# Kernel tuning notes

Hardware: AMD Instinct MI355X
Metric: run time of the kernel (lower is better)

Reference implementation:

```python
import jax, jax.numpy as jnp
import numpy as np

B, S, J, D = 64, 2048, 25, 3
FEAT_DIM = 128
COMPUTED = 12  # pos(3) + vel(3) + acc(3) + angles(3)
IN_MLP = COMPUTED * J  # 300
HID = FEAT_DIM * 2     # 256
CONN = np.array([(0, 1), (1, 5), (1, 6), (5, 7), (7, 9), (6, 8), (8, 10),
                 (1, 11), (1, 12), (11, 13), (13, 15), (12, 14), (14, 16)], dtype=np.int32)


def setup_inputs() -> dict:
    key = jax.random.key(0)
    ks = jax.random.split(key, 8)
    return {
        "poses": jax.random.normal(ks[0], (B, S, J, D), dtype=jnp.float32),
        "W1": jax.random.normal(ks[1], (IN_MLP, HID), dtype=jnp.float32) * 0.05,
        "b1": jnp.zeros((HID,), jnp.float32),
        "gamma": jnp.ones((HID,), jnp.float32),
        "beta": jnp.zeros((HID,), jnp.float32),
        "running_mean": jnp.zeros((HID,), jnp.float32),
        "running_var": jnp.ones((HID,), jnp.float32),
        "W2": jax.random.normal(ks[2], (HID, FEAT_DIM), dtype=jnp.float32) * 0.05,
        "b2": jnp.zeros((FEAT_DIM,), jnp.float32),
        "joint_weights": jnp.ones((J,), jnp.float32),
    }


def reference(poses, W1, b1, gamma, beta, running_mean, running_var, W2, b2, joint_weights):
    b, s, j, d = poses.shape
    # --- root-centering + max-distance normalization ---
    p = poses - poses[:, :, 0:1, :]
    dist = jnp.linalg.norm(p, axis=-1, keepdims=True)           # [B,S,J,1]
    max_dist = jnp.max(dist, axis=2, keepdims=True)             # [B,S,1,1]
    p = p / (max_dist + 1e-8)
    # --- velocity / acceleration (zero-padded first frames) ---
    zpad = jnp.zeros_like(p[:, :1])
    vel = jnp.concatenate([zpad, p[:, 1:] - p[:, :-1]], axis=1)
    acc = jnp.concatenate([zpad, vel[:, 1:] - vel[:, :-1]], axis=1)
    # --- joint angles: vectorized gather + normalize + acos (replaces B*S*13 python loop) ---
    v1 = p[:, :, CONN[:, 1], :] - p[:, :, CONN[:, 0], :]        # [B,S,13,3]
    vnorm = jnp.maximum(jnp.linalg.norm(v1, axis=-1, keepdims=True), 1e-12)  # F.normalize eps
    ang = jnp.arccos(jnp.clip(v1 / vnorm, -1.0, 1.0))           # [B,S,13,3]
    ang = ang.reshape(b, s, -1)                                 # [B,S,39]
    pad = jnp.zeros((b, s, j * 3 - ang.shape[-1]), ang.dtype)   # pad to J*3=75
    angles = jnp.concatenate([ang, pad], axis=-1).reshape(b, s, j, 3)
    # --- combine, weight, project ---
    feat = jnp.concatenate([p, vel, acc, angles], axis=-1)      # [B,S,J,12]
    feat = feat * joint_weights.reshape(1, 1, j, 1)
    x = feat.reshape(b * s, -1)                                 # [B*S,300]
    x = x @ W1 + b1
    x = gamma * (x - running_mean) / jnp.sqrt(running_var + 1e-5) + beta  # BN eval mode
    x = jax.nn.relu(x)                                          # dropout = identity (eval)
    x = x @ W2 + b2
    return x.reshape(b, s, -1)                                  # [B,S,128]
```

## Files before the change

kernel.cpp:

```cpp
#include <hip/hip_runtime.h>
#include <hip/hip_bf16.h>
#include <stdint.h>


#define S_    2048
#define MT_   64
#define TPB   512
#define HID_  256
#define OUT_  128

typedef __attribute__((ext_vector_type(8))) short   short8;
typedef __attribute__((ext_vector_type(4))) float   floatx4;

#define C0M 0x0ECDB118675110ULL
#define C1M 0x0FDECBA9786540ULL

__device__ __forceinline__ unsigned short bf16_bits(float v) {
    union { float f; unsigned u; } x; x.f = v;
    unsigned r = x.u + 0x7fffu + ((x.u >> 16) & 1u);
    return (unsigned short)(r >> 16);
}

__device__ __forceinline__ unsigned pkbf16(float a, float b) {
#if __has_builtin(__builtin_amdgcn_cvt_pk_bf16_f32)
    auto v = __builtin_amdgcn_cvt_pk_bf16_f32(a, b);
    unsigned u; __builtin_memcpy(&u, &v, 4); return u;
#else
    return (unsigned)bf16_bits(a) | ((unsigned)bf16_bits(b) << 16);
#endif
}

__device__ __forceinline__ float facos(float x) {
    float ax = fabsf(x);
    float p = fmaf(ax, -0.0187293f, 0.0742610f);
    p = fmaf(ax, p, -0.2121144f);
    p = fmaf(ax, p, 1.5707288f);
    float r = __builtin_amdgcn_sqrtf(1.f - ax) * p;
    return x < 0.f ? 3.14159265358979f - r : r;
}

__global__ void prep_kernel(const float* __restrict__ W1, const float* __restrict__ b1,
                            const float* __restrict__ gamma, const float* __restrict__ beta,
                            const float* __restrict__ rmean, const float* __restrict__ rvar,
                            const float* __restrict__ W2,
                            unsigned short* __restrict__ w1p,
                            unsigned short* __restrict__ w2p,
                            float* __restrict__ b1p) {
    int idx = blockIdx.x * 256 + threadIdx.x;
    if (idx < 81920) {
        int k = idx >> 8, n = idx & 255;
        float a = gamma[n] * __builtin_amdgcn_rsqf(rvar[n] + 1e-5f);
        float v = (k < 300) ? W1[k * HID_ + n] * a : 0.f;
        int blk = (k >> 5) * 16 + (n >> 4);
        int off = blk * 512 + (((k >> 3) & 3) * 16 + (n & 15)) * 8 + (k & 7);
        w1p[off] = bf16_bits(v);
    } else if (idx < 114688) {
        int i2 = idx - 81920;
        int k = i2 >> 7, n = i2 & 127;
        int blk = (k >> 5) * 8 + (n >> 4);
        int off = blk * 512 + (((k >> 3) & 3) * 16 + (n & 15)) * 8 + (k & 7);
        w2p[off] = bf16_bits(W2[k * OUT_ + n]);
    } else if (idx < 114944) {
        int n = idx - 114688;
        float a = gamma[n] * __builtin_amdgcn_rsqf(rvar[n] + 1e-5f);
        b1p[n] = fmaf(a, b1[n] - rmean[n], beta[n]);
    }
}

#define LDS_FEAT 0
#define LDS_PM   41984
#define LDS_RS   43312
#define LDS_JW   (LDS_RS + 66 * 16)
#define LDS_TOT  (LDS_JW + 25 * 4 + 12)

__global__ __launch_bounds__(TPB, 6) void pose_mlp(
    const float* __restrict__ poses,
    const unsigned short* __restrict__ w1p,
    const unsigned short* __restrict__ w2p,
    const float* __restrict__ b1p,
    const float* __restrict__ b2,
    const float* __restrict__ jw,
    float* __restrict__ out)
{
    __shared__ __align__(16) unsigned char smem[LDS_TOT];
    const int tid  = threadIdx.x;
    const int lane = tid & 63;
    const int wv   = tid >> 6;
    const int t0   = blockIdx.x * MT_;
    const int s0   = t0 & (S_ - 1);

    unsigned short* feat = (unsigned short*)(smem + LDS_FEAT);
    float*  pm  = (float*)(smem + LDS_PM);
    float4* rs  = (float4*)(smem + LDS_RS);
    float*  jwl = (float*)(smem + LDS_JW);

    short8 bw[2];
    #pragma unroll
    for (int ni = 0; ni < 2; ni++)
        bw[ni] = *(const short8*)(w1p + (unsigned)(wv * 2 + ni) * 512 + lane * 8);

    if (tid < 25) jwl[tid] = jw[tid];
    for (int i = tid; i < MT_ * 64; i += TPB) {
        int tt = i >> 6, z = i & 63;
        int k;
        if (z < 36) { int jj = z / 3; k = (13 + jj) * 12 + 9 + (z - jj * 3); }
        else        { k = 300 + z - 36; }
        feat[tt * 328 + k] = 0;
    }

    for (int i = tid; i < 66 * 5; i += TPB) {
        int f = i / 5, grp = i - f * 5;
        int g = t0 - 2 + f; if (g < 0) g = 0;
        const float* P = poses + (size_t)g * 75;
        float r0 = P[0], r1 = P[1], r2 = P[2];
        float m2 = 0.f;
        #pragma unroll
        for (int jj = 0; jj < 5; jj++) {
            int j = grp * 5 + jj;
            float dx = P[j*3]   - r0;
            float dy = P[j*3+1] - r1;
            float dz = P[j*3+2] - r2;
            m2 = fmaxf(m2, fmaf(dx, dx, fmaf(dy, dy, dz * dz)));
        }
        pm[i] = m2;
    }
    __syncthreads();
    if (tid < 66) {
        int g = t0 - 2 + tid; if (g < 0) g = 0;
        const float* P = poses + (size_t)g * 75;
        const float* q = pm + tid * 5;
        float m2 = fmaxf(fmaxf(fmaxf(q[0], q[1]), fmaxf(q[2], q[3])), q[4]);
        float sc = __builtin_amdgcn_rcpf(__builtin_amdgcn_sqrtf(m2) + 1e-8f);
        rs[tid] = make_float4(P[0], P[1], P[2], sc);
    }
    __syncthreads();

    for (int i = tid; i < MT_ * 25; i += TPB) {
        int tt = i / 25, j = i - tt * 25;
        int s  = s0 + tt;
        int g  = t0 + tt;
        int g1 = g - 1 < 0 ? 0 : g - 1;
        int g2 = g - 2 < 0 ? 0 : g - 2;
        const float* Pc = poses + (size_t)g  * 75 + j * 3;
        const float* P1 = poses + (size_t)g1 * 75 + j * 3;
        const float* P2 = poses + (size_t)g2 * 75 + j * 3;
        float4 rc = rs[tt + 2], rm = rs[tt + 1], rp = rs[tt];
        float cx = (Pc[0] - rc.x) * rc.w, cy = (Pc[1] - rc.y) * rc.w, cz = (Pc[2] - rc.z) * rc.w;
        float mx = (P1[0] - rm.x) * rm.w, my = (P1[1] - rm.y) * rm.w, mz = (P1[2] - rm.z) * rm.w;
        float px = (P2[0] - rp.x) * rp.w, py = (P2[1] - rp.y) * rp.w, pz = (P2[2] - rp.z) * rp.w;
        bool h1 = (s >= 1), h2 = (s >= 2);
        float vx = h1 ? cx - mx : 0.f, vy = h1 ? cy - my : 0.f, vz = h1 ? cz - mz : 0.f;
        float ux = h2 ? mx - px : 0.f, uy = h2 ? my - py : 0.f, uz = h2 ? mz - pz : 0.f;
        float qx = vx - ux, qy = vy - uy, qz = vz - uz;
        float w = jwl[j];
        unsigned base = (unsigned)tt * 328 + j * 12;
        *(unsigned*)(feat + base)     = pkbf16(cx * w, cy * w);
        *(unsigned*)(feat + base + 2) = pkbf16(cz * w, vx * w);
        *(unsigned*)(feat + base + 4) = pkbf16(vy * w, vz * w);
        *(unsigned*)(feat + base + 6) = pkbf16(qx * w, qy * w);
        feat[base + 8] = bf16_bits(qz * w);
    }

    for (int i = tid; i < MT_ * 13; i += TPB) {
        int tt = i / 13, e = i - tt * 13;
        int g  = t0 + tt;
        const float* P = poses + (size_t)g * 75;
        int a0 = (int)((C0M >> (4 * e)) & 15) * 3;
        int a1 = (((int)((C1M >> (4 * e)) & 15)) + 1) * 3;
        float vx = P[a1] - P[a0], vy = P[a1+1] - P[a0+1], vz = P[a1+2] - P[a0+2];
        float d  = fmaf(vx, vx, fmaf(vy, vy, vz * vz));
        float inv = __builtin_amdgcn_rcpf(fmaxf(__builtin_amdgcn_sqrtf(d), 1e-12f));
        float w = jwl[e];
        float A0 = facos(fminf(fmaxf(vx * inv, -1.f), 1.f)) * w;
        float A1 = facos(fminf(fmaxf(vy * inv, -1.f), 1.f)) * w;
        float A2 = facos(fminf(fmaxf(vz * inv, -1.f), 1.f)) * w;
        unsigned base = (unsigned)tt * 328 + e * 12 + 9;
        feat[base] = bf16_bits(A0);
        *(unsigned*)(feat + base + 1) = pkbf16(A1, A2);
    }
    __syncthreads();

    floatx4 acc[4][2];
    #pragma unroll
    for (int mi = 0; mi < 4; mi++)
        #pragma unroll
        for (int ni = 0; ni < 2; ni++) acc[mi][ni] = (floatx4){0.f, 0.f, 0.f, 0.f};

    #pragma unroll 1
    for (int kc = 0; kc < 10; kc++) {
        short8 bn[2];
        if (kc < 9) {
            #pragma unroll
            for (int ni = 0; ni < 2; ni++)
                bn[ni] = *(const short8*)(w1p + (unsigned)((kc + 1) * 16 + wv * 2 + ni) * 512 + lane * 8);
        }
        short8 af[4];
        #pragma unroll
        for (int mi = 0; mi < 4; mi++)
            af[mi] = *(const short8*)(feat + (mi * 16 + (lane & 15)) * 328 + kc * 32 + (lane >> 4) * 8);
        #pragma unroll
        for (int mi = 0; mi < 4; mi++)
            #pragma unroll
            for (int ni = 0; ni < 2; ni++)
                acc[mi][ni] = __builtin_amdgcn_mfma_f32_16x16x32_bf16(
                    af[mi], bw[ni], acc[mi][ni], 0, 0, 0);
        if (kc < 9) {
            #pragma unroll
            for (int ni = 0; ni < 2; ni++) bw[ni] = bn[ni];
        }
    }

    short8 bw2 = *(const short8*)(w2p + (unsigned)wv * 512 + lane * 8);

    __syncthreads();

    unsigned short* hid = feat;
    float bv[2];
    #pragma unroll
    for (int ni = 0; ni < 2; ni++) bv[ni] = b1p[wv * 32 + ni * 16 + (lane & 15)];
    #pragma unroll
    for (int mi = 0; mi < 4; mi++)
        #pragma unroll
        for (int ni = 0; ni < 2; ni++)
            #pragma unroll
            for (int r = 0; r < 4; r++) {
                float v = fmaxf(acc[mi][ni][r] + bv[ni], 0.f);
                int m   = mi * 16 + (lane >> 4) * 4 + r;
                int col = wv * 32 + ni * 16 + (lane & 15);
                hid[m * 264 + col] = bf16_bits(v);
            }
    __syncthreads();

    floatx4 acc2[4];
    #pragma unroll
    for (int mi = 0; mi < 4; mi++) acc2[mi] = (floatx4){0.f, 0.f, 0.f, 0.f};

    #pragma unroll 1
    for (int kc = 0; kc < 8; kc++) {
        short8 bn2;
        if (kc < 7)
            bn2 = *(const short8*)(w2p + (unsigned)((kc + 1) * 8 + wv) * 512 + lane * 8);
        short8 af[4];
        #pragma unroll
        for (int mi = 0; mi < 4; mi++)
            af[mi] = *(const short8*)(hid + (mi * 16 + (lane & 15)) * 264 + kc * 32 + (lane >> 4) * 8);
        #pragma unroll
        for (int mi = 0; mi < 4; mi++)
            acc2[mi] = __builtin_amdgcn_mfma_f32_16x16x32_bf16(
                af[mi], bw2, acc2[mi], 0, 0, 0);
        if (kc < 7) bw2 = bn2;
    }

    float c2 = b2[wv * 16 + (lane & 15)];
    #pragma unroll
    for (int mi = 0; mi < 4; mi++)
        #pragma unroll
        for (int r = 0; r < 4; r++) {
            int m   = mi * 16 + (lane >> 4) * 4 + r;
            int col = wv * 16 + (lane & 15);
            out[(size_t)(t0 + m) * OUT_ + col] = acc2[mi][r] + c2;
        }
}

extern "C" void kernel_launch(void* const* d_in, const int* in_sizes, int n_in,
                              void* d_out, int out_size, void* d_ws, size_t ws_size,
                              hipStream_t stream) {
    (void)in_sizes; (void)n_in; (void)out_size; (void)ws_size;
    const float* poses = (const float*)d_in[0];
    const float* W1    = (const float*)d_in[1];
    const float* b1    = (const float*)d_in[2];
    const float* gamma = (const float*)d_in[3];
    const float* beta  = (const float*)d_in[4];
    const float* rmean = (const float*)d_in[5];
    const float* rvar  = (const float*)d_in[6];
    const float* W2    = (const float*)d_in[7];
    const float* b2    = (const float*)d_in[8];
    const float* jw    = (const float*)d_in[9];

    unsigned short* w1p = (unsigned short*)d_ws;
    unsigned short* w2p = w1p + 320 * HID_;
    float* b1p = (float*)((char*)d_ws + (320 * HID_ + HID_ * OUT_) * 2);

    prep_kernel<<<449, 256, 0, stream>>>(W1, b1, gamma, beta, rmean, rvar, W2,
                                         w1p, w2p, b1p);
    pose_mlp<<<2048, TPB, 0, stream>>>(poses, w1p, w2p, b1p, b2, jw, (float*)d_out);
}
```

Measured before the change: 144.4 us.

## Fold velocity/acceleration and joint weights into W1, feed shifted normalized poses

Velocity and acceleration are linear in the normalized positions of the current and two previous frames, so their W1 rows are folded into three combined weight groups. The GEMM now reads time-shifted rows of a compact normalized-pose tile. Joint weights are also moved into the weight prep. This removes per-element vel/acc feature construction and shrinks the LDS footprint, allowing 8 blocks per CU instead of 6. The cost is K growing from 320 to 352 (11 MFMA k-chunks instead of 10). Zero-padding at sequence starts is now reproduced by clamping to the first frame, so the differences come out as zero.

```diff
diff --git a/kernel.cpp b/kernel.cpp
--- a/kernel.cpp
+++ b/kernel.cpp
@@ -8,6 +8,7 @@
 #define TPB   512
 #define HID_  256
 #define OUT_  128
+#define NK1   11
 
 typedef __attribute__((ext_vector_type(8))) short   short8;
 typedef __attribute__((ext_vector_type(4))) float   floatx4;
@@ -42,44 +43,63 @@
 __global__ void prep_kernel(const float* __restrict__ W1, const float* __restrict__ b1,
                             const float* __restrict__ gamma, const float* __restrict__ beta,
                             const float* __restrict__ rmean, const float* __restrict__ rvar,
-                            const float* __restrict__ W2,
+                            const float* __restrict__ W2, const float* __restrict__ jw,
                             unsigned short* __restrict__ w1p,
                             unsigned short* __restrict__ w2p,
                             float* __restrict__ b1p) {
     int idx = blockIdx.x * 256 + threadIdx.x;
-    if (idx < 81920) {
+    if (idx < 352 * 256) {
         int k = idx >> 8, n = idx & 255;
         float a = gamma[n] * __builtin_amdgcn_rsqf(rvar[n] + 1e-5f);
-        float v = (k < 300) ? W1[k * HID_ + n] * a : 0.f;
+        float v = 0.f;
+        if (k < 288) {
+            int g = k / 96, kk = k - g * 96;
+            if (kk < 75) {
+                int j = kk / 3, c = kk - j * 3;
+                int base = (j * 12 + c) * HID_ + n;
+                float wp = W1[base];
+                float wv = W1[base + 3 * HID_];
+                float wa = W1[base + 6 * HID_];
+                float m  = jw[j] * a;
+                v = (g == 0 ? (wp + wv + wa) : (g == 1 ? -(wv + 2.f * wa) : wa)) * m;
+            }
+        } else {
+            int kk = k - 288;
+            if (kk < 39) {
+                int j = kk / 3, c = kk - j * 3;
+                v = W1[(j * 12 + 9 + c) * HID_ + n] * jw[j] * a;
+            }
+        }
         int blk = (k >> 5) * 16 + (n >> 4);
         int off = blk * 512 + (((k >> 3) & 3) * 16 + (n & 15)) * 8 + (k & 7);
         w1p[off] = bf16_bits(v);
-    } else if (idx < 114688) {
-        int i2 = idx - 81920;
+    } else if (idx < 352 * 256 + 256 * 128) {
+        int i2 = idx - 352 * 256;
         int k = i2 >> 7, n = i2 & 127;
         int blk = (k >> 5) * 8 + (n >> 4);
         int off = blk * 512 + (((k >> 3) & 3) * 16 + (n & 15)) * 8 + (k & 7);
         w2p[off] = bf16_bits(W2[k * OUT_ + n]);
-    } else if (idx < 114944) {
-        int n = idx - 114688;
+    } else if (idx < 352 * 256 + 256 * 128 + 256) {
+        int n = idx - (352 * 256 + 256 * 128);
         float a = gamma[n] * __builtin_amdgcn_rsqf(rvar[n] + 1e-5f);
         b1p[n] = fmaf(a, b1[n] - rmean[n], beta[n]);
     }
 }
 
-#define LDS_FEAT 0
-#define LDS_PM   41984
-#define LDS_RS   43312
-#define LDS_JW   (LDS_RS + 66 * 16)
-#define LDS_TOT  (LDS_JW + 25 * 4 + 12)
-
-__global__ __launch_bounds__(TPB, 6) void pose_mlp(
+#define PT_STR   100
+#define ANG_STR  72
+#define HID_STR  268
+#define LDS_ANG  13216
+#define LDS_PM   22432
+#define LDS_RS   23760
+#define LDS_TOT  (64 * HID_STR * 2)
+
+__global__ __launch_bounds__(TPB, 8) void pose_mlp(
     const float* __restrict__ poses,
     const unsigned short* __restrict__ w1p,
     const unsigned short* __restrict__ w2p,
     const float* __restrict__ b1p,
     const float* __restrict__ b2,
-    const float* __restrict__ jw,
     float* __restrict__ out)
 {
     __shared__ __align__(16) unsigned char smem[LDS_TOT];
@@ -89,28 +109,19 @@
     const int t0   = blockIdx.x * MT_;
     const int s0   = t0 & (S_ - 1);
 
-    unsigned short* feat = (unsigned short*)(smem + LDS_FEAT);
-    float*  pm  = (float*)(smem + LDS_PM);
-    float4* rs  = (float4*)(smem + LDS_RS);
-    float*  jwl = (float*)(smem + LDS_JW);
+    unsigned short* pt  = (unsigned short*)smem;
+    unsigned short* ang = (unsigned short*)(smem + LDS_ANG);
+    float*  pm = (float*)(smem + LDS_PM);
+    float4* rs = (float4*)(smem + LDS_RS);
 
     short8 bw[2];
     #pragma unroll
     for (int ni = 0; ni < 2; ni++)
         bw[ni] = *(const short8*)(w1p + (unsigned)(wv * 2 + ni) * 512 + lane * 8);
 
-    if (tid < 25) jwl[tid] = jw[tid];
-    for (int i = tid; i < MT_ * 64; i += TPB) {
-        int tt = i >> 6, z = i & 63;
-        int k;
-        if (z < 36) { int jj = z / 3; k = (13 + jj) * 12 + 9 + (z - jj * 3); }
-        else        { k = 300 + z - 36; }
-        feat[tt * 328 + k] = 0;
-    }
-
     for (int i = tid; i < 66 * 5; i += TPB) {
         int f = i / 5, grp = i - f * 5;
-        int g = t0 - 2 + f; if (g < 0) g = 0;
+        int g = (s0 - 2 + f < 0) ? t0 : t0 - 2 + f;
         const float* P = poses + (size_t)g * 75;
         float r0 = P[0], r1 = P[1], r2 = P[2];
         float m2 = 0.f;
@@ -126,7 +137,7 @@
     }
     __syncthreads();
     if (tid < 66) {
-        int g = t0 - 2 + tid; if (g < 0) g = 0;
+        int g = (s0 - 2 + tid < 0) ? t0 : t0 - 2 + tid;
         const float* P = poses + (size_t)g * 75;
         const float* q = pm + tid * 5;
         float m2 = fmaxf(fmaxf(fmaxf(q[0], q[1]), fmaxf(q[2], q[3])), q[4]);
@@ -135,48 +146,46 @@
     }
     __syncthreads();
 
-    for (int i = tid; i < MT_ * 25; i += TPB) {
-        int tt = i / 25, j = i - tt * 25;
-        int s  = s0 + tt;
-        int g  = t0 + tt;
-        int g1 = g - 1 < 0 ? 0 : g - 1;
-        int g2 = g - 2 < 0 ? 0 : g - 2;
-        const float* Pc = poses + (size_t)g  * 75 + j * 3;
-        const float* P1 = poses + (size_t)g1 * 75 + j * 3;
-        const float* P2 = poses + (size_t)g2 * 75 + j * 3;
-        float4 rc = rs[tt + 2], rm = rs[tt + 1], rp = rs[tt];
-        float cx = (Pc[0] - rc.x) * rc.w, cy = (Pc[1] - rc.y) * rc.w, cz = (Pc[2] - rc.z) * rc.w;
-        float mx = (P1[0] - rm.x) * rm.w, my = (P1[1] - rm.y) * rm.w, mz = (P1[2] - rm.z) * rm.w;
-        float px = (P2[0] - rp.x) * rp.w, py = (P2[1] - rp.y) * rp.w, pz = (P2[2] - rp.z) * rp.w;
-        bool h1 = (s >= 1), h2 = (s >= 2);
-        float vx = h1 ? cx - mx : 0.f, vy = h1 ? cy - my : 0.f, vz = h1 ? cz - mz : 0.f;
-        float ux = h2 ? mx - px : 0.f, uy = h2 ? my - py : 0.f, uz = h2 ? mz - pz : 0.f;
-        float qx = vx - ux, qy = vy - uy, qz = vz - uz;
-        float w = jwl[j];
-        unsigned base = (unsigned)tt * 328 + j * 12;
-        *(unsigned*)(feat + base)     = pkbf16(cx * w, cy * w);
-        *(unsigned*)(feat + base + 2) = pkbf16(cz * w, vx * w);
-        *(unsigned*)(feat + base + 4) = pkbf16(vy * w, vz * w);
-        *(unsigned*)(feat + base + 6) = pkbf16(qx * w, qy * w);
-        feat[base + 8] = bf16_bits(qz * w);
+    for (int i = tid; i < 66 * 50; i += TPB) {
+        int f = i / 50, p = i - f * 50;
+        int r0 = 2 * p, r1 = r0 + 1;
+        int g = (s0 - 2 + f < 0) ? t0 : t0 - 2 + f;
+        const float* P = poses + (size_t)g * 75;
+        float4 R = rs[f];
+        float v0 = 0.f, v1 = 0.f;
+        if (r0 < 75) {
+            int c = r0 - (r0 / 3) * 3;
+            float rt = (c == 0) ? R.x : ((c == 1) ? R.y : R.z);
+            v0 = (P[r0] - rt) * R.w;
+        }
+        if (r1 < 75) {
+            int c = r1 - (r1 / 3) * 3;
+            float rt = (c == 0) ? R.x : ((c == 1) ? R.y : R.z);
+            v1 = (P[r1] - rt) * R.w;
+        }
+        *(unsigned*)(pt + f * PT_STR + r0) = pkbf16(v0, v1);
     }
 
     for (int i = tid; i < MT_ * 13; i += TPB) {
         int tt = i / 13, e = i - tt * 13;
-        int g  = t0 + tt;
-        const float* P = poses + (size_t)g * 75;
+        const float* P = poses + (size_t)(t0 + tt) * 75;
         int a0 = (int)((C0M >> (4 * e)) & 15) * 3;
         int a1 = (((int)((C1M >> (4 * e)) & 15)) + 1) * 3;
         float vx = P[a1] - P[a0], vy = P[a1+1] - P[a0+1], vz = P[a1+2] - P[a0+2];
         float d  = fmaf(vx, vx, fmaf(vy, vy, vz * vz));
         float inv = __builtin_amdgcn_rcpf(fmaxf(__builtin_amdgcn_sqrtf(d), 1e-12f));
-        float w = jwl[e];
-        float A0 = facos(fminf(fmaxf(vx * inv, -1.f), 1.f)) * w;
-        float A1 = facos(fminf(fmaxf(vy * inv, -1.f), 1.f)) * w;
-        float A2 = facos(fminf(fmaxf(vz * inv, -1.f), 1.f)) * w;
-        unsigned base = (unsigned)tt * 328 + e * 12 + 9;
-        feat[base] = bf16_bits(A0);
-        *(unsigned*)(feat + base + 1) = pkbf16(A1, A2);
+        float A0 = facos(fminf(fmaxf(vx * inv, -1.f), 1.f));
+        float A1 = facos(fminf(fmaxf(vy * inv, -1.f), 1.f));
+        float A2 = facos(fminf(fmaxf(vz * inv, -1.f), 1.f));
+        unsigned base = (unsigned)tt * ANG_STR + e * 3;
+        ang[base]     = bf16_bits(A0);
+        ang[base + 1] = bf16_bits(A1);
+        ang[base + 2] = bf16_bits(A2);
+    }
+    for (int i = tid; i < MT_ * 13; i += TPB) {
+        int r = i / 13, q = i - r * 13;
+        if (q == 0) ang[r * ANG_STR + 39] = 0;
+        else *(unsigned*)(ang + r * ANG_STR + 40 + 2 * (q - 1)) = 0;
     }
     __syncthreads();
 
@@ -187,24 +196,35 @@
         for (int ni = 0; ni < 2; ni++) acc[mi][ni] = (floatx4){0.f, 0.f, 0.f, 0.f};
 
     #pragma unroll 1
-    for (int kc = 0; kc < 10; kc++) {
+    for (int kc = 0; kc < NK1; kc++) {
         short8 bn[2];
-        if (kc < 9) {
+        if (kc < NK1 - 1) {
             #pragma unroll
             for (int ni = 0; ni < 2; ni++)
                 bn[ni] = *(const short8*)(w1p + (unsigned)((kc + 1) * 16 + wv * 2 + ni) * 512 + lane * 8);
         }
         short8 af[4];
-        #pragma unroll
-        for (int mi = 0; mi < 4; mi++)
-            af[mi] = *(const short8*)(feat + (mi * 16 + (lane & 15)) * 328 + kc * 32 + (lane >> 4) * 8);
+        if (kc < 9) {
+            int grp = kc / 3;
+            int ko  = (kc - grp * 3) * 32 + (lane >> 4) * 8;
+            #pragma unroll
+            for (int mi = 0; mi < 4; mi++) {
+                int row = mi * 16 + (lane & 15) + 2 - grp;
+                af[mi] = *(const short8*)(pt + row * PT_STR + ko);
+            }
+        } else {
+            int ko = (kc - 9) * 32 + (lane >> 4) * 8;
+            #pragma unroll
+            for (int mi = 0; mi < 4; mi++)
+                af[mi] = *(const short8*)(ang + (mi * 16 + (lane & 15)) * ANG_STR + ko);
+        }
         #pragma unroll
         for (int mi = 0; mi < 4; mi++)
             #pragma unroll
             for (int ni = 0; ni < 2; ni++)
                 acc[mi][ni] = __builtin_amdgcn_mfma_f32_16x16x32_bf16(
                     af[mi], bw[ni], acc[mi][ni], 0, 0, 0);
-        if (kc < 9) {
+        if (kc < NK1 - 1) {
             #pragma unroll
             for (int ni = 0; ni < 2; ni++) bw[ni] = bn[ni];
         }
@@ -214,7 +234,7 @@
 
     __syncthreads();
 
-    unsigned short* hid = feat;
+    unsigned short* hid = (unsigned short*)smem;
     float bv[2];
     #pragma unroll
     for (int ni = 0; ni < 2; ni++) bv[ni] = b1p[wv * 32 + ni * 16 + (lane & 15)];
@@ -227,7 +247,7 @@
                 float v = fmaxf(acc[mi][ni][r] + bv[ni], 0.f);
                 int m   = mi * 16 + (lane >> 4) * 4 + r;
                 int col = wv * 32 + ni * 16 + (lane & 15);
-                hid[m * 264 + col] = bf16_bits(v);
+                hid[m * HID_STR + col] = bf16_bits(v);
             }
     __syncthreads();
 
@@ -243,7 +263,7 @@
         short8 af[4];
         #pragma unroll
         for (int mi = 0; mi < 4; mi++)
-            af[mi] = *(const short8*)(hid + (mi * 16 + (lane & 15)) * 264 + kc * 32 + (lane >> 4) * 8);
+            af[mi] = *(const short8*)(hid + (mi * 16 + (lane & 15)) * HID_STR + kc * 32 + (lane >> 4) * 8);
         #pragma unroll
         for (int mi = 0; mi < 4; mi++)
             acc2[mi] = __builtin_amdgcn_mfma_f32_16x16x32_bf16(
@@ -278,10 +298,10 @@
     const float* jw    = (const float*)d_in[9];
 
     unsigned short* w1p = (unsigned short*)d_ws;
-    unsigned short* w2p = w1p + 320 * HID_;
-    float* b1p = (float*)((char*)d_ws + (320 * HID_ + HID_ * OUT_) * 2);
-
-    prep_kernel<<<449, 256, 0, stream>>>(W1, b1, gamma, beta, rmean, rvar, W2,
+    unsigned short* w2p = w1p + 352 * HID_;
+    float* b1p = (float*)((char*)d_ws + (352 * HID_ + HID_ * OUT_) * 2);
+
+    prep_kernel<<<481, 256, 0, stream>>>(W1, b1, gamma, beta, rmean, rvar, W2, jw,
                                          w1p, w2p, b1p);
-    pose_mlp<<<2048, TPB, 0, stream>>>(poses, w1p, w2p, b1p, b2, jw, (float*)d_out);
-}
+    pose_mlp<<<2048, TPB, 0, stream>>>(poses, w1p, w2p, b1p, b2, (float*)d_out);
+}
```

After: 238.9 us. 65.4% more time.
